# Kernel optimization log

Hardware: AMD Instinct MI355X
Metric: run time of the kernel (lower is better)

Reference implementation:

```python
import jax, jax.numpy as jnp
import numpy as np

B, S, D, H = 4, 2048, 1024, 16
HD = D // H


def setup_inputs() -> dict:
    key = jax.random.key(0)
    ks = jax.random.split(key, 12)
    scale = 1.0 / np.sqrt(D)
    inp = {
        "query": jax.random.normal(ks[0], (B, S, D), jnp.float32),
        "key_": jax.random.normal(ks[1], (B, S, D), jnp.float32),
        "value": jax.random.normal(ks[2], (B, S, D), jnp.float32),
        "Wq": jax.random.normal(ks[3], (D, D), jnp.float32) * scale,
        "bq": jnp.zeros((D,), jnp.float32),
        "Wk": jax.random.normal(ks[4], (D, D), jnp.float32) * scale,
        "bk": jnp.zeros((D,), jnp.float32),
        "Wv": jax.random.normal(ks[5], (D, D), jnp.float32) * scale,
        "bv": jnp.zeros((D,), jnp.float32),
        "Wo": jax.random.normal(ks[6], (D, D), jnp.float32) * scale,
        "bo": jnp.zeros((D,), jnp.float32),
        # causal mask: 1 where attention allowed, 0 where masked (masked_fill(mask==0, -inf))
        "mask": jnp.tril(jnp.ones((S, S), jnp.int32))[None, None, :, :],
    }
    return inp


def reference(query, key_, value, Wq, bq, Wk, bk, Wv, bv, Wo, bo, mask):
    def split_heads(x):  # [B,S,D] -> [B,H,S,HD]
        return x.reshape(B, S, H, HD).transpose(0, 2, 1, 3)

    Q = split_heads(query @ Wq.T + bq)
    K = split_heads(key_ @ Wk.T + bk)
    V = split_heads(value @ Wv.T + bv)

    scores = jnp.einsum("bhqd,bhkd->bhqk", Q, K) / np.sqrt(HD).astype(np.float32)
    scores = jnp.where(mask == 0, -jnp.inf, scores)
    attn = jax.nn.softmax(scores, axis=-1)  # [B,H,S,S]
    out = jnp.einsum("bhqk,bhkd->bhqd", attn, V)  # [B,H,S,HD]
    concat = out.transpose(0, 2, 1, 3).reshape(B, S, D)
    return concat @ Wo.T + bo
```

## Files before the change

kernel.cpp:

```cpp
#include <hip/hip_runtime.h>
#include <hip/hip_bf16.h>
#include <math.h>

#define BB 4
#define SS 2048
#define DD 1024
#define HH 16
#define HD 64

#define NEG_BIG (-1e30f)


typedef short v8s __attribute__((ext_vector_type(8)));
typedef float v4f __attribute__((ext_vector_type(4)));

__device__ inline unsigned cvt_pk_bf16(float lo, float hi) {
    unsigned r;
    asm("v_cvt_pk_bf16_f32 %0, %1, %2" : "=v"(r) : "v"(lo), "v"(hi));
    return r;
}

__device__ inline short f2bf(float f) {
    return (short)cvt_pk_bf16(f, f);
}

__device__ inline v4f v4f_zero() {
    v4f z;
    z[0] = 0.f; z[1] = 0.f; z[2] = 0.f; z[3] = 0.f;
    return z;
}

__device__ inline v8s load8f(const float* p) {
    v4f a = *(const v4f*)p;
    v4f b = *(const v4f*)(p + 4);
    union { unsigned u[4]; v8s s; } x;
    x.u[0] = cvt_pk_bf16(a[0], a[1]);
    x.u[1] = cvt_pk_bf16(a[2], a[3]);
    x.u[2] = cvt_pk_bf16(b[0], b[1]);
    x.u[3] = cvt_pk_bf16(b[2], b[3]);
    return x.s;
}

__device__ inline void gll16(const void* g, void* l) {
    __builtin_amdgcn_global_load_lds(
        (const __attribute__((address_space(1))) unsigned*)g,
        (__attribute__((address_space(3))) unsigned*)l, 16, 0, 0);
}

__global__ __launch_bounds__(256) void conv_bf16_kernel(
    const float* __restrict__ in, short* __restrict__ out, int n8) {
    int i = blockIdx.x * 256 + threadIdx.x;
    const int stride = gridDim.x * 256;
    for (; i < n8; i += stride) {
        *((v8s*)out + i) = load8f(in + (size_t)i * 8);
    }
}

template <int MODE>
__global__ __launch_bounds__(256) void gemm_kernel(
    const void* __restrict__ Pbig, const float* __restrict__ Psml,
    const float* __restrict__ Pbias, void* __restrict__ PC,
    const void* __restrict__ Pbig2, const float* __restrict__ Psml2,
    const float* __restrict__ Pbias2, void* __restrict__ PC2) {
    __shared__ short sA[128 * 32];
    __shared__ short sB[128 * 32];

    const int tid = threadIdx.x;
    const int lane = tid & 63;
    const int wave = tid >> 6;
    const int quad = lane >> 4;
    const int l16 = lane & 15;
    const int wm = wave >> 1;
    const int wn = wave & 1;

    const void* Big = Pbig;
    const float* Sml = Psml;
    const float* bias = Pbias;
    void* Cv = PC;
    if (MODE == 0 && blockIdx.z == 1) {
        Big = Pbig2; Sml = Psml2; bias = Pbias2; Cv = PC2;
    }

    int bx = blockIdx.x, by = blockIdx.y;
    if (MODE != 1) {
        int b = bx + (by << 3);
        int l = ((b & 7) << 6) + (b >> 3);
        bx = l & 7;
        by = l >> 3;
    }
    const int m0 = by * 128;
    const int n0 = bx * 128;

    short* sBig = (MODE == 1) ? sB : sA;
    short* sSml = (MODE == 1) ? sA : sB;
    const int grow = (wave << 5) + (lane >> 2);
    const int gcol = (lane & 3) << 3;
    const short* BigS = (const short*)Big;
    size_t gbase0, gbase1;
    if (MODE == 3) {
        int ma = m0 + grow, mb = m0 + grow + 16;
        gbase0 = ((size_t)((ma >> 11) * HH) * SS + (ma & 2047)) * HD;
        gbase1 = ((size_t)((mb >> 11) * HH) * SS + (mb & 2047)) * HD;
    } else {
        int r0 = ((MODE == 1) ? n0 : m0) + grow;
        gbase0 = (size_t)r0 * 1024 + gcol;
        gbase1 = gbase0 + (size_t)16 * 1024;
    }
    short* ldst0 = sBig + (wave << 10);
    short* ldst1 = ldst0 + 512;

    const int sml_base = (MODE == 1) ? m0 : n0;

    v4f acc[4][4];
#pragma unroll
    for (int i = 0; i < 4; i++)
#pragma unroll
        for (int j = 0; j < 4; j++) acc[i][j] = v4f_zero();

    for (int k0 = 0; k0 < 1024; k0 += 32) {
        __syncthreads();
        if (MODE == 3) {
            size_t hoff = (size_t)(k0 >> 6) * (SS * HD) + (k0 & 63) + gcol;
            gll16(BigS + gbase0 + hoff, ldst0);
            gll16(BigS + gbase1 + hoff, ldst1);
        } else {
            gll16(BigS + gbase0 + k0, ldst0);
            gll16(BigS + gbase1 + k0, ldst1);
        }
#pragma unroll
        for (int p = 0; p < 2; p++) {
            int idx = ((p << 8) + tid) << 3;
            int r = idx >> 5;
            int c = idx & 31;
            *(v8s*)&sSml[idx] =
                load8f(Sml + (size_t)(sml_base + r) * 1024 + k0 + c);
        }
        __syncthreads();

        v8s af[4], bfr[4];
#pragma unroll
        for (int i = 0; i < 4; i++)
            af[i] = *(const v8s*)&sA[(wm * 64 + i * 16 + l16) * 32 + quad * 8];
#pragma unroll
        for (int j = 0; j < 4; j++)
            bfr[j] = *(const v8s*)&sB[(wn * 64 + j * 16 + l16) * 32 + quad * 8];
#pragma unroll
        for (int i = 0; i < 4; i++)
#pragma unroll
            for (int j = 0; j < 4; j++)
                acc[i][j] = __builtin_amdgcn_mfma_f32_16x16x32_bf16(
                    af[i], bfr[j], acc[i][j], 0, 0, 0);
    }

#pragma unroll
    for (int i = 0; i < 4; i++) {
#pragma unroll
        for (int j = 0; j < 4; j++) {
#pragma unroll
            for (int r = 0; r < 4; r++) {
                int ml = wm * 64 + i * 16 + quad * 4 + r;
                int nl = wn * 64 + j * 16 + l16;
                int m = m0 + ml;
                int n = n0 + nl;
                float v = acc[i][j][r];
                if (MODE == 0) {
                    v += bias[n];
                    int b = m >> 11, s = m & 2047, h = n >> 6, d = n & 63;
                    ((short*)Cv)[(((size_t)(b * HH + h) * SS + s) << 6) + d] =
                        f2bf(v);
                } else if (MODE == 1) {
                    v += bias[m];
                    int h = m >> 6, d = m & 63, b = n >> 11, s = n & 2047;
                    ((short*)Cv)[((size_t)(b * HH + h) * HD + d) * SS + s] =
                        f2bf(v);
                } else {
                    v += bias[n];
                    ((float*)Cv)[(size_t)m * 1024 + n] = v;
                }
            }
        }
    }
}

__global__ __launch_bounds__(256) void attn_kernel(
    short* __restrict__ QO, const short* __restrict__ Kt,
    const short* __restrict__ Vt) {
    constexpr int LDR = 64 + 8;
    __shared__ short sK[64 * LDR];
    __shared__ short sV[64 * LDR];
    __shared__ short sP[4][16 * LDR];

    const int tid = threadIdx.x;
    const int lane = tid & 63;
    const int wave = tid >> 6;
    const int quad = lane >> 4;
    const int l16 = lane & 15;
    const int qt = (int)gridDim.x - 1 - (int)blockIdx.x;
    const int bh = blockIdx.y;

    short* Qh = QO + (size_t)bh * SS * HD;
    const short* Kh = Kt + (size_t)bh * SS * HD;
    const short* Vh = Vt + (size_t)bh * HD * SS;

    const int qrow = qt * 64 + wave * 16 + l16;
    v8s qf[2];
    qf[0] = *(const v8s*)&Qh[(size_t)qrow * HD + quad * 8];
    qf[1] = *(const v8s*)&Qh[(size_t)qrow * HD + 32 + quad * 8];

    v8s onesb;
#pragma unroll
    for (int i = 0; i < 8; i++) onesb[i] = (short)0x3F80;

    v4f o[4];
#pragma unroll
    for (int j = 0; j < 4; j++) o[j] = v4f_zero();
    v4f oSum = v4f_zero();
    float mOld[4];
#pragma unroll
    for (int r = 0; r < 4; r++) mOld[r] = NEG_BIG;

    const int qg_base = qt * 64 + wave * 16 + quad * 4;

    for (int kt = 0; kt <= qt; kt++) {
        __syncthreads();
#pragma unroll
        for (int p = 0; p < 2; p++) {
            int idx = (p * 256 + tid) * 8;
            int r = idx >> 6;
            int c = idx & 63;
            *(v8s*)&sK[r * LDR + c] =
                *(const v8s*)&Kh[(size_t)(kt * 64 + r) * HD + c];
            *(v8s*)&sV[r * LDR + c] =
                *(const v8s*)&Vh[(size_t)r * SS + kt * 64 + c];
        }
        __syncthreads();

        __builtin_amdgcn_s_setprio(1);
        v4f sc[4];
#pragma unroll
        for (int j = 0; j < 4; j++) {
            v8s b0 = *(const v8s*)&sK[(j * 16 + l16) * LDR + quad * 8];
            v8s b1 = *(const v8s*)&sK[(j * 16 + l16) * LDR + 32 + quad * 8];
            v4f t = __builtin_amdgcn_mfma_f32_16x16x32_bf16(qf[0], b0,
                                                            v4f_zero(), 0, 0, 0);
            sc[j] = __builtin_amdgcn_mfma_f32_16x16x32_bf16(qf[1], b1, t, 0, 0, 0);
        }
        __builtin_amdgcn_s_setprio(0);

        float x[4][4];
        const bool diag = (kt == qt);
#pragma unroll
        for (int j = 0; j < 4; j++) {
#pragma unroll
            for (int r = 0; r < 4; r++) {
                float v = sc[j][r] * 0.125f;
                if (diag) {
                    int kg = kt * 64 + j * 16 + l16;
                    int qg = qg_base + r;
                    if (kg > qg) v = NEG_BIG;
                }
                x[j][r] = v;
            }
        }

        float mNew[4], alpha[4];
#pragma unroll
        for (int r = 0; r < 4; r++) {
            float t = fmaxf(fmaxf(x[0][r], x[1][r]), fmaxf(x[2][r], x[3][r]));
#pragma unroll
            for (int off = 8; off >= 1; off >>= 1) t = fmaxf(t, __shfl_xor(t, off));
            mNew[r] = fmaxf(mOld[r], t);
            alpha[r] = __expf(mOld[r] - mNew[r]);
            mOld[r] = mNew[r];
        }

        short* Pw = sP[wave];
#pragma unroll
        for (int j = 0; j < 4; j++)
#pragma unroll
            for (int r = 0; r < 4; r++) {
                float p = __expf(x[j][r] - mNew[r]);
                Pw[(quad * 4 + r) * LDR + j * 16 + l16] = f2bf(p);
            }
#pragma unroll
        for (int j = 0; j < 4; j++)
#pragma unroll
            for (int r = 0; r < 4; r++) o[j][r] *= alpha[r];
#pragma unroll
        for (int r = 0; r < 4; r++) oSum[r] *= alpha[r];

        v8s pa0 = *(const v8s*)&Pw[l16 * LDR + quad * 8];
        v8s pa1 = *(const v8s*)&Pw[l16 * LDR + 32 + quad * 8];
        __builtin_amdgcn_s_setprio(1);
#pragma unroll
        for (int j = 0; j < 4; j++) {
            v8s v0 = *(const v8s*)&sV[(j * 16 + l16) * LDR + quad * 8];
            v8s v1 = *(const v8s*)&sV[(j * 16 + l16) * LDR + 32 + quad * 8];
            o[j] = __builtin_amdgcn_mfma_f32_16x16x32_bf16(pa0, v0, o[j], 0, 0, 0);
            o[j] = __builtin_amdgcn_mfma_f32_16x16x32_bf16(pa1, v1, o[j], 0, 0, 0);
        }
        oSum = __builtin_amdgcn_mfma_f32_16x16x32_bf16(pa0, onesb, oSum, 0, 0, 0);
        oSum = __builtin_amdgcn_mfma_f32_16x16x32_bf16(pa1, onesb, oSum, 0, 0, 0);
        __builtin_amdgcn_s_setprio(0);
    }

#pragma unroll
    for (int r = 0; r < 4; r++) {
        float inv = 1.f / oSum[r];
        int s = qg_base + r;
#pragma unroll
        for (int j = 0; j < 4; j++) {
            float v = o[j][r] * inv;
            Qh[(size_t)s * HD + j * 16 + l16] = f2bf(v);
        }
    }
}

extern "C" void kernel_launch(void* const* d_in, const int* in_sizes, int n_in,
                              void* d_out, int out_size, void* d_ws, size_t ws_size,
                              hipStream_t stream) {
    const float* query = (const float*)d_in[0];
    const float* key_ = (const float*)d_in[1];
    const float* value = (const float*)d_in[2];
    const float* Wq = (const float*)d_in[3];
    const float* bq = (const float*)d_in[4];
    const float* Wk = (const float*)d_in[5];
    const float* bk = (const float*)d_in[6];
    const float* Wv = (const float*)d_in[7];
    const float* bv = (const float*)d_in[8];
    const float* Wo = (const float*)d_in[9];
    const float* bo = (const float*)d_in[10];
    float* out = (float*)d_out;

    const size_t NE = (size_t)BB * SS * DD;

    short* qx = (short*)d_out;
    short* kx = (short*)d_out + NE;
    short* vx = (short*)d_out + NE;
    short* vw = (short*)d_out;
    short* qw = (short*)d_ws;
    short* kw = (short*)d_ws + NE;

    dim3 blk(256);
    const int n8 = (int)(NE / 8);
    conv_bf16_kernel<<<dim3(2048), blk, 0, stream>>>(query, qx, n8);
    conv_bf16_kernel<<<dim3(2048), blk, 0, stream>>>(key_, kx, n8);
    gemm_kernel<0><<<dim3(8, 64, 2), blk, 0, stream>>>(
        qx, Wq, bq, qw, kx, Wk, bk, kw);
    conv_bf16_kernel<<<dim3(2048), blk, 0, stream>>>(value, vx, n8);
    gemm_kernel<1><<<dim3(64, 8), blk, 0, stream>>>(
        vx, Wv, bv, vw, nullptr, nullptr, nullptr, nullptr);
    attn_kernel<<<dim3(SS / 64, BB * HH), blk, 0, stream>>>(qw, kw, vw);
    gemm_kernel<3><<<dim3(8, 64), blk, 0, stream>>>(
        qw, Wo, bo, out, nullptr, nullptr, nullptr, nullptr);
}
```

Baseline: 508.7 us.

## Double-buffer GEMM and attention tiles, widen attention to 128 queries per block

The GEMM kernel gains double-buffered shared tiles: the next K-slice (global_load_lds for activations, register-staged weights) is prefetched while MFMAs run on the current slice, and the MFMA loop gets raised priority. The MODE 1 grid is remapped for XCD locality, and the V output is written with a permuted sequence order so attention can store P as packed 4-element vectors. The attention kernel now handles 128 query rows per block (two 16-row groups per wave), which reuses each K/V tile across twice as many queries and halves the grid. It also double-buffers the K/V tiles with register prefetch. The costs are more registers and shared memory, which may reduce occupancy, plus finer-grained causal masking logic.

```diff
diff --git a/kernel.cpp b/kernel.cpp
--- a/kernel.cpp
+++ b/kernel.cpp
@@ -13,6 +13,7 @@
 
 typedef short v8s __attribute__((ext_vector_type(8)));
 typedef float v4f __attribute__((ext_vector_type(4)));
+typedef unsigned v2u __attribute__((ext_vector_type(2)));
 
 __device__ inline unsigned cvt_pk_bf16(float lo, float hi) {
     unsigned r;
@@ -30,9 +31,7 @@
     return z;
 }
 
-__device__ inline v8s load8f(const float* p) {
-    v4f a = *(const v4f*)p;
-    v4f b = *(const v4f*)(p + 4);
+__device__ inline v8s cvt8(v4f a, v4f b) {
     union { unsigned u[4]; v8s s; } x;
     x.u[0] = cvt_pk_bf16(a[0], a[1]);
     x.u[1] = cvt_pk_bf16(a[2], a[3]);
@@ -41,6 +40,10 @@
     return x.s;
 }
 
+__device__ inline v8s load8f(const float* p) {
+    return cvt8(*(const v4f*)p, *(const v4f*)(p + 4));
+}
+
 __device__ inline void gll16(const void* g, void* l) {
     __builtin_amdgcn_global_load_lds(
         (const __attribute__((address_space(1))) unsigned*)g,
@@ -62,8 +65,8 @@
     const float* __restrict__ Pbias, void* __restrict__ PC,
     const void* __restrict__ Pbig2, const float* __restrict__ Psml2,
     const float* __restrict__ Pbias2, void* __restrict__ PC2) {
-    __shared__ short sA[128 * 32];
-    __shared__ short sB[128 * 32];
+    __shared__ short sA[2][128 * 32];
+    __shared__ short sB[2][128 * 32];
 
     const int tid = threadIdx.x;
     const int lane = tid & 63;
@@ -81,18 +84,21 @@
         Big = Pbig2; Sml = Psml2; bias = Pbias2; Cv = PC2;
     }
 
-    int bx = blockIdx.x, by = blockIdx.y;
+    int bx, by;
     if (MODE != 1) {
-        int b = bx + (by << 3);
+        int b = blockIdx.x + (blockIdx.y << 3);
         int l = ((b & 7) << 6) + (b >> 3);
         bx = l & 7;
         by = l >> 3;
+    } else {
+        int L = blockIdx.x + blockIdx.y * 64;
+        int xcd = L & 7, slot = L >> 3;
+        bx = xcd * 8 + (slot & 7);
+        by = slot >> 3;
     }
     const int m0 = by * 128;
     const int n0 = bx * 128;
 
-    short* sBig = (MODE == 1) ? sB : sA;
-    short* sSml = (MODE == 1) ? sA : sB;
     const int grow = (wave << 5) + (lane >> 2);
     const int gcol = (lane & 3) << 3;
     const short* BigS = (const short*)Big;
@@ -106,10 +112,12 @@
         gbase0 = (size_t)r0 * 1024 + gcol;
         gbase1 = gbase0 + (size_t)16 * 1024;
     }
-    short* ldst0 = sBig + (wave << 10);
-    short* ldst1 = ldst0 + 512;
+    const int ldoff = wave << 10;
 
     const int sml_base = (MODE == 1) ? m0 : n0;
+    const int idx0 = tid << 3, idx1 = (256 + tid) << 3;
+    const float* Wsrc0 = Sml + (size_t)(sml_base + (idx0 >> 5)) * 1024 + (idx0 & 31);
+    const float* Wsrc1 = Sml + (size_t)(sml_base + (idx1 >> 5)) * 1024 + (idx1 & 31);
 
     v4f acc[4][4];
 #pragma unroll
@@ -117,39 +125,67 @@
 #pragma unroll
         for (int j = 0; j < 4; j++) acc[i][j] = v4f_zero();
 
-    for (int k0 = 0; k0 < 1024; k0 += 32) {
+    {
+        short* sBigT = (MODE == 1) ? sB[0] : sA[0];
+        short* sSmlT = (MODE == 1) ? sA[0] : sB[0];
+        if (MODE == 3) {
+            size_t hoff = (size_t)gcol;
+            gll16(BigS + gbase0 + hoff, sBigT + ldoff);
+            gll16(BigS + gbase1 + hoff, sBigT + ldoff + 512);
+        } else {
+            gll16(BigS + gbase0, sBigT + ldoff);
+            gll16(BigS + gbase1, sBigT + ldoff + 512);
+        }
+        v4f w00 = *(const v4f*)Wsrc0, w01 = *(const v4f*)(Wsrc0 + 4);
+        v4f w10 = *(const v4f*)Wsrc1, w11 = *(const v4f*)(Wsrc1 + 4);
+        *(v8s*)&sSmlT[idx0] = cvt8(w00, w01);
+        *(v8s*)&sSmlT[idx1] = cvt8(w10, w11);
+    }
+
+    int cur = 0;
+    for (int k0 = 0; k0 < 1024; k0 += 32, cur ^= 1) {
         __syncthreads();
-        if (MODE == 3) {
-            size_t hoff = (size_t)(k0 >> 6) * (SS * HD) + (k0 & 63) + gcol;
-            gll16(BigS + gbase0 + hoff, ldst0);
-            gll16(BigS + gbase1 + hoff, ldst1);
-        } else {
-            gll16(BigS + gbase0 + k0, ldst0);
-            gll16(BigS + gbase1 + k0, ldst1);
-        }
-#pragma unroll
-        for (int p = 0; p < 2; p++) {
-            int idx = ((p << 8) + tid) << 3;
-            int r = idx >> 5;
-            int c = idx & 31;
-            *(v8s*)&sSml[idx] =
-                load8f(Sml + (size_t)(sml_base + r) * 1024 + k0 + c);
-        }
-        __syncthreads();
+
+        const int k1 = k0 + 32;
+        const bool pre = (k1 < 1024);
+        v4f w00, w01, w10, w11;
+        if (pre) {
+            short* sBigN = (MODE == 1) ? sB[cur ^ 1] : sA[cur ^ 1];
+            if (MODE == 3) {
+                size_t hoff = (size_t)(k1 >> 6) * (SS * HD) + (k1 & 63) + gcol;
+                gll16(BigS + gbase0 + hoff, sBigN + ldoff);
+                gll16(BigS + gbase1 + hoff, sBigN + ldoff + 512);
+            } else {
+                gll16(BigS + gbase0 + k1, sBigN + ldoff);
+                gll16(BigS + gbase1 + k1, sBigN + ldoff + 512);
+            }
+            w00 = *(const v4f*)(Wsrc0 + k1);
+            w01 = *(const v4f*)(Wsrc0 + k1 + 4);
+            w10 = *(const v4f*)(Wsrc1 + k1);
+            w11 = *(const v4f*)(Wsrc1 + k1 + 4);
+        }
 
         v8s af[4], bfr[4];
 #pragma unroll
         for (int i = 0; i < 4; i++)
-            af[i] = *(const v8s*)&sA[(wm * 64 + i * 16 + l16) * 32 + quad * 8];
+            af[i] = *(const v8s*)&sA[cur][(wm * 64 + i * 16 + l16) * 32 + quad * 8];
 #pragma unroll
         for (int j = 0; j < 4; j++)
-            bfr[j] = *(const v8s*)&sB[(wn * 64 + j * 16 + l16) * 32 + quad * 8];
+            bfr[j] = *(const v8s*)&sB[cur][(wn * 64 + j * 16 + l16) * 32 + quad * 8];
+        __builtin_amdgcn_s_setprio(1);
 #pragma unroll
         for (int i = 0; i < 4; i++)
 #pragma unroll
             for (int j = 0; j < 4; j++)
                 acc[i][j] = __builtin_amdgcn_mfma_f32_16x16x32_bf16(
                     af[i], bfr[j], acc[i][j], 0, 0, 0);
+        __builtin_amdgcn_s_setprio(0);
+
+        if (pre) {
+            short* sSmlN = (MODE == 1) ? sA[cur ^ 1] : sB[cur ^ 1];
+            *(v8s*)&sSmlN[idx0] = cvt8(w00, w01);
+            *(v8s*)&sSmlN[idx1] = cvt8(w10, w11);
+        }
     }
 
 #pragma unroll
@@ -171,7 +207,8 @@
                 } else if (MODE == 1) {
                     v += bias[m];
                     int h = m >> 6, d = m & 63, b = n >> 11, s = n & 2047;
-                    ((short*)Cv)[((size_t)(b * HH + h) * HD + d) * SS + s] =
+                    int sp = (s & ~63) | ((s & 15) << 2) | ((s >> 4) & 3);
+                    ((short*)Cv)[((size_t)(b * HH + h) * HD + d) * SS + sp] =
                         f2bf(v);
                 } else {
                     v += bias[n];
@@ -185,9 +222,9 @@
 __global__ __launch_bounds__(256) void attn_kernel(
     short* __restrict__ QO, const short* __restrict__ Kt,
     const short* __restrict__ Vt) {
-    constexpr int LDR = 64 + 8;
-    __shared__ short sK[64 * LDR];
-    __shared__ short sV[64 * LDR];
+    constexpr int LDR = 72;
+    __shared__ short sK[2][64 * LDR];
+    __shared__ short sV[2][64 * LDR];
     __shared__ short sP[4][16 * LDR];
 
     const int tid = threadIdx.x;
@@ -202,116 +239,168 @@
     const short* Kh = Kt + (size_t)bh * SS * HD;
     const short* Vh = Vt + (size_t)bh * HD * SS;
 
-    const int qrow = qt * 64 + wave * 16 + l16;
-    v8s qf[2];
-    qf[0] = *(const v8s*)&Qh[(size_t)qrow * HD + quad * 8];
-    qf[1] = *(const v8s*)&Qh[(size_t)qrow * HD + 32 + quad * 8];
+    const int srow = tid >> 3;
+    const int scol = (tid & 7) << 3;
+
+    const int qbase = qt * 128 + wave * 32;
+    v8s qf[2][2];
+#pragma unroll
+    for (int g = 0; g < 2; g++) {
+        const short* qp = &Qh[(size_t)(qbase + g * 16 + l16) * HD];
+        qf[g][0] = *(const v8s*)&qp[quad * 8];
+        qf[g][1] = *(const v8s*)&qp[32 + quad * 8];
+    }
 
     v8s onesb;
 #pragma unroll
     for (int i = 0; i < 8; i++) onesb[i] = (short)0x3F80;
 
-    v4f o[4];
-#pragma unroll
-    for (int j = 0; j < 4; j++) o[j] = v4f_zero();
-    v4f oSum = v4f_zero();
-    float mOld[4];
-#pragma unroll
-    for (int r = 0; r < 4; r++) mOld[r] = NEG_BIG;
-
-    const int qg_base = qt * 64 + wave * 16 + quad * 4;
-
-    for (int kt = 0; kt <= qt; kt++) {
+    v4f o[2][4];
+#pragma unroll
+    for (int g = 0; g < 2; g++)
+#pragma unroll
+        for (int j = 0; j < 4; j++) o[g][j] = v4f_zero();
+    v4f oSum[2];
+    oSum[0] = v4f_zero();
+    oSum[1] = v4f_zero();
+    float mOld[2][4];
+#pragma unroll
+    for (int g = 0; g < 2; g++)
+#pragma unroll
+        for (int r = 0; r < 4; r++) mOld[g][r] = NEG_BIG;
+
+    const int ktmax = 2 * qt + 1;
+
+    {
+        v8s a0 = *(const v8s*)&Kh[(size_t)srow * HD + scol];
+        v8s a1 = *(const v8s*)&Kh[(size_t)(srow + 32) * HD + scol];
+        v8s b0 = *(const v8s*)&Vh[(size_t)srow * SS + scol];
+        v8s b1 = *(const v8s*)&Vh[(size_t)(srow + 32) * SS + scol];
+        *(v8s*)&sK[0][srow * LDR + scol] = a0;
+        *(v8s*)&sK[0][(srow + 32) * LDR + scol] = a1;
+        *(v8s*)&sV[0][srow * LDR + scol] = b0;
+        *(v8s*)&sV[0][(srow + 32) * LDR + scol] = b1;
+    }
+
+    int cur = 0;
+    for (int kt = 0; kt <= ktmax; kt++, cur ^= 1) {
         __syncthreads();
-#pragma unroll
-        for (int p = 0; p < 2; p++) {
-            int idx = (p * 256 + tid) * 8;
-            int r = idx >> 6;
-            int c = idx & 63;
-            *(v8s*)&sK[r * LDR + c] =
-                *(const v8s*)&Kh[(size_t)(kt * 64 + r) * HD + c];
-            *(v8s*)&sV[r * LDR + c] =
-                *(const v8s*)&Vh[(size_t)r * SS + kt * 64 + c];
-        }
-        __syncthreads();
-
+
+        const bool pre = (kt < ktmax);
+        v8s pk0, pk1, pv0, pv1;
+        if (pre) {
+            int kb = (kt + 1) * 64;
+            pk0 = *(const v8s*)&Kh[(size_t)(kb + srow) * HD + scol];
+            pk1 = *(const v8s*)&Kh[(size_t)(kb + srow + 32) * HD + scol];
+            pv0 = *(const v8s*)&Vh[(size_t)srow * SS + kb + scol];
+            pv1 = *(const v8s*)&Vh[(size_t)(srow + 32) * SS + kb + scol];
+        }
+
+        v4f sc[2][4];
         __builtin_amdgcn_s_setprio(1);
-        v4f sc[4];
 #pragma unroll
         for (int j = 0; j < 4; j++) {
-            v8s b0 = *(const v8s*)&sK[(j * 16 + l16) * LDR + quad * 8];
-            v8s b1 = *(const v8s*)&sK[(j * 16 + l16) * LDR + 32 + quad * 8];
-            v4f t = __builtin_amdgcn_mfma_f32_16x16x32_bf16(qf[0], b0,
-                                                            v4f_zero(), 0, 0, 0);
-            sc[j] = __builtin_amdgcn_mfma_f32_16x16x32_bf16(qf[1], b1, t, 0, 0, 0);
+            v8s b0 = *(const v8s*)&sK[cur][(j * 16 + l16) * LDR + quad * 8];
+            v8s b1 = *(const v8s*)&sK[cur][(j * 16 + l16) * LDR + 32 + quad * 8];
+#pragma unroll
+            for (int g = 0; g < 2; g++) {
+                v4f t = __builtin_amdgcn_mfma_f32_16x16x32_bf16(
+                    qf[g][0], b0, v4f_zero(), 0, 0, 0);
+                sc[g][j] = __builtin_amdgcn_mfma_f32_16x16x32_bf16(
+                    qf[g][1], b1, t, 0, 0, 0);
+            }
         }
         __builtin_amdgcn_s_setprio(0);
 
-        float x[4][4];
-        const bool diag = (kt == qt);
-#pragma unroll
-        for (int j = 0; j < 4; j++) {
+#pragma unroll
+        for (int g = 0; g < 2; g++) {
+            const int gb = qbase + g * 16;
+            const int qgb = gb + quad * 4;
+            const bool gate = (kt * 64 + 63) > gb;
+            float x[4][4];
+#pragma unroll
+            for (int j = 0; j < 4; j++) {
+#pragma unroll
+                for (int r = 0; r < 4; r++) {
+                    float v = sc[g][j][r] * 0.125f;
+                    if (gate) {
+                        int kg = kt * 64 + j * 16 + l16;
+                        if (kg > qgb + r) v = NEG_BIG;
+                    }
+                    x[j][r] = v;
+                }
+            }
+
+            float mNew[4], alpha[4];
 #pragma unroll
             for (int r = 0; r < 4; r++) {
-                float v = sc[j][r] * 0.125f;
-                if (diag) {
-                    int kg = kt * 64 + j * 16 + l16;
-                    int qg = qg_base + r;
-                    if (kg > qg) v = NEG_BIG;
-                }
-                x[j][r] = v;
-            }
-        }
-
-        float mNew[4], alpha[4];
+                float t = fmaxf(fmaxf(x[0][r], x[1][r]), fmaxf(x[2][r], x[3][r]));
+#pragma unroll
+                for (int off = 8; off >= 1; off >>= 1)
+                    t = fmaxf(t, __shfl_xor(t, off));
+                mNew[r] = fmaxf(mOld[g][r], t);
+                alpha[r] = __expf(mOld[g][r] - mNew[r]);
+                mOld[g][r] = mNew[r];
+            }
+
+            short* Pw = sP[wave];
+#pragma unroll
+            for (int r = 0; r < 4; r++) {
+                float p0 = __expf(x[0][r] - mNew[r]);
+                float p1 = __expf(x[1][r] - mNew[r]);
+                float p2 = __expf(x[2][r] - mNew[r]);
+                float p3 = __expf(x[3][r] - mNew[r]);
+                v2u w;
+                w[0] = cvt_pk_bf16(p0, p1);
+                w[1] = cvt_pk_bf16(p2, p3);
+                *(v2u*)&Pw[(quad * 4 + r) * LDR + l16 * 4] = w;
+            }
+#pragma unroll
+            for (int j = 0; j < 4; j++)
+#pragma unroll
+                for (int r = 0; r < 4; r++) o[g][j][r] *= alpha[r];
+#pragma unroll
+            for (int r = 0; r < 4; r++) oSum[g][r] *= alpha[r];
+
+            v8s pa0 = *(const v8s*)&Pw[l16 * LDR + quad * 8];
+            v8s pa1 = *(const v8s*)&Pw[l16 * LDR + 32 + quad * 8];
+            __builtin_amdgcn_s_setprio(1);
+#pragma unroll
+            for (int j = 0; j < 4; j++) {
+                v8s v0 = *(const v8s*)&sV[cur][(j * 16 + l16) * LDR + quad * 8];
+                v8s v1 = *(const v8s*)&sV[cur][(j * 16 + l16) * LDR + 32 + quad * 8];
+                o[g][j] = __builtin_amdgcn_mfma_f32_16x16x32_bf16(
+                    pa0, v0, o[g][j], 0, 0, 0);
+                o[g][j] = __builtin_amdgcn_mfma_f32_16x16x32_bf16(
+                    pa1, v1, o[g][j], 0, 0, 0);
+            }
+            oSum[g] = __builtin_amdgcn_mfma_f32_16x16x32_bf16(
+                pa0, onesb, oSum[g], 0, 0, 0);
+            oSum[g] = __builtin_amdgcn_mfma_f32_16x16x32_bf16(
+                pa1, onesb, oSum[g], 0, 0, 0);
+            __builtin_amdgcn_s_setprio(0);
+        }
+
+        if (pre) {
+            int nxt = cur ^ 1;
+            *(v8s*)&sK[nxt][srow * LDR + scol] = pk0;
+            *(v8s*)&sK[nxt][(srow + 32) * LDR + scol] = pk1;
+            *(v8s*)&sV[nxt][srow * LDR + scol] = pv0;
+            *(v8s*)&sV[nxt][(srow + 32) * LDR + scol] = pv1;
+        }
+    }
+
+#pragma unroll
+    for (int g = 0; g < 2; g++) {
 #pragma unroll
         for (int r = 0; r < 4; r++) {
-            float t = fmaxf(fmaxf(x[0][r], x[1][r]), fmaxf(x[2][r], x[3][r]));
-#pragma unroll
-            for (int off = 8; off >= 1; off >>= 1) t = fmaxf(t, __shfl_xor(t, off));
-            mNew[r] = fmaxf(mOld[r], t);
-            alpha[r] = __expf(mOld[r] - mNew[r]);
-            mOld[r] = mNew[r];
-        }
-
-        short* Pw = sP[wave];
-#pragma unroll
-        for (int j = 0; j < 4; j++)
-#pragma unroll
-            for (int r = 0; r < 4; r++) {
-                float p = __expf(x[j][r] - mNew[r]);
-                Pw[(quad * 4 + r) * LDR + j * 16 + l16] = f2bf(p);
-            }
-#pragma unroll
-        for (int j = 0; j < 4; j++)
-#pragma unroll
-            for (int r = 0; r < 4; r++) o[j][r] *= alpha[r];
-#pragma unroll
-        for (int r = 0; r < 4; r++) oSum[r] *= alpha[r];
-
-        v8s pa0 = *(const v8s*)&Pw[l16 * LDR + quad * 8];
-        v8s pa1 = *(const v8s*)&Pw[l16 * LDR + 32 + quad * 8];
-        __builtin_amdgcn_s_setprio(1);
-#pragma unroll
-        for (int j = 0; j < 4; j++) {
-            v8s v0 = *(const v8s*)&sV[(j * 16 + l16) * LDR + quad * 8];
-            v8s v1 = *(const v8s*)&sV[(j * 16 + l16) * LDR + 32 + quad * 8];
-            o[j] = __builtin_amdgcn_mfma_f32_16x16x32_bf16(pa0, v0, o[j], 0, 0, 0);
-            o[j] = __builtin_amdgcn_mfma_f32_16x16x32_bf16(pa1, v1, o[j], 0, 0, 0);
-        }
-        oSum = __builtin_amdgcn_mfma_f32_16x16x32_bf16(pa0, onesb, oSum, 0, 0, 0);
-        oSum = __builtin_amdgcn_mfma_f32_16x16x32_bf16(pa1, onesb, oSum, 0, 0, 0);
-        __builtin_amdgcn_s_setprio(0);
-    }
-
-#pragma unroll
-    for (int r = 0; r < 4; r++) {
-        float inv = 1.f / oSum[r];
-        int s = qg_base + r;
-#pragma unroll
-        for (int j = 0; j < 4; j++) {
-            float v = o[j][r] * inv;
-            Qh[(size_t)s * HD + j * 16 + l16] = f2bf(v);
+            float inv = 1.f / oSum[g][r];
+            int s = qbase + g * 16 + quad * 4 + r;
+#pragma unroll
+            for (int j = 0; j < 4; j++) {
+                float v = o[g][j][r] * inv;
+                Qh[(size_t)s * HD + j * 16 + l16] = f2bf(v);
+            }
         }
     }
 }
@@ -350,7 +439,7 @@
     conv_bf16_kernel<<<dim3(2048), blk, 0, stream>>>(value, vx, n8);
     gemm_kernel<1><<<dim3(64, 8), blk, 0, stream>>>(
         vx, Wv, bv, vw, nullptr, nullptr, nullptr, nullptr);
-    attn_kernel<<<dim3(SS / 64, BB * HH), blk, 0, stream>>>(qw, kw, vw);
+    attn_kernel<<<dim3(SS / 128, BB * HH), blk, 0, stream>>>(qw, kw, vw);
     gemm_kernel<3><<<dim3(8, 64), blk, 0, stream>>>(
         qw, Wo, bo, out, nullptr, nullptr, nullptr, nullptr);
 }
```

Result: slower. 553.5 us (+8.8%).
